# Performance work log

Hardware: AMD Instinct MI355X
Metric: run time of the kernel (lower is better)

Reference implementation:

```python
import jax, jax.numpy as jnp
import numpy as np

N, HEADS, OUT = 8192, 4, 64  # hidden = HEADS*OUT = 256
DIN = 256
NEG = -9e15
ALPHA = 0.2


def setup_inputs() -> dict:
    key = jax.random.key(0)
    ks = jax.random.split(key, 6)
    X = jax.random.normal(ks[0], (N, DIN), dtype=jnp.float32)
    A = jax.random.randint(ks[1], (N, N), 0, 2, dtype=jnp.int32)  # dense 0/1 adjacency
    hid = HEADS * OUT
    W = jax.random.normal(ks[2], (hid, DIN), dtype=jnp.float32) * 0.05  # nn.Linear weight [out,in]
    b = jax.random.normal(ks[3], (hid,), dtype=jnp.float32) * 0.05
    a_s = jax.random.normal(ks[4], (hid, 1), dtype=jnp.float32) * 0.05
    a_r = jax.random.normal(ks[5], (hid, 1), dtype=jnp.float32) * 0.05
    return {"X": X, "A": A, "W": W, "b": b, "a_s": a_s, "a_r": a_r}


def reference(X, A, W, b, a_s, a_r):
    Af = A.astype(jnp.float32)
    H_in = X @ W.T + b                      # [N, hid]
    s = H_in @ a_s                          # [N, 1]
    r = H_in @ a_r                          # [N, 1]
    M = Af * s + Af * r.T                   # M_s + M_r, [N, N]
    scores = jax.nn.leaky_relu(M, negative_slope=ALPHA)
    masked = jnp.where(Af > 0, scores, jnp.float32(NEG))
    C = jax.nn.softmax(masked, axis=1)      # row softmax; dropout = identity (eval)
    H_out = C @ H_in                        # [N, hid]; act = Identity, LayerNorm output discarded
    H_final = H_out.reshape(N, HEADS, OUT).sum(axis=1)  # concat='sum'
    return H_final
```

## Files before the change

### kernel.cpp

```cpp
#include <hip/hip_runtime.h>

typedef __attribute__((ext_vector_type(8))) short short8;
typedef __attribute__((ext_vector_type(4))) short short4v;
typedef __attribute__((ext_vector_type(4))) float f32x4;
typedef __attribute__((ext_vector_type(4))) int i32x4;

#define NN 8192
#define ALPHA 0.2f

__device__ __forceinline__ float bf16_to_f32(unsigned short h) {
    union { unsigned int u; float f; } c;
    c.u = ((unsigned int)h) << 16;
    return c.f;
}
__device__ __forceinline__ unsigned short f32_to_bf16(float f) {
    union { float f; unsigned int u; } c;
    c.f = f;
    unsigned int r = (c.u + 0x7FFFu + ((c.u >> 16) & 1u)) >> 16;
    return (unsigned short)r;
}
__device__ __forceinline__ unsigned short f32_to_bf16_fast(float f) {
    union { float f; unsigned int u; } c;
    c.f = f;
    return (unsigned short)((c.u + 0x8000u) >> 16);
}

__global__ void gat_probe_dtype(const unsigned short* __restrict__ x16, int* flag) {
    __shared__ int cnts[256];
    int tid = threadIdx.x;
    int cnt = 0;
    for (int i = tid; i < 16384; i += 256) {
        float v = bf16_to_f32(x16[i]);
        float a = fabsf(v);
        if (a > 1e-6f && a < 64.0f) cnt++;
    }
    cnts[tid] = cnt;
    __syncthreads();
    for (int s = 128; s > 0; s >>= 1) {
        if (tid < s) cnts[tid] += cnts[tid + s];
        __syncthreads();
    }
    if (tid == 0) *flag = (cnts[0] > 13000) ? 1 : 0;
}

__global__ void gat_convert(const void* __restrict__ Xv, const void* __restrict__ Wv,
                            const void* __restrict__ bv, const void* __restrict__ asv,
                            const void* __restrict__ arv,
                            short* __restrict__ Xb, short* __restrict__ Wb,
                            float* __restrict__ bF, float* __restrict__ asF,
                            float* __restrict__ arF, const int* __restrict__ flag) {
    const int GX = NN * 256 / 8;
    const int GW = 256 * 256 / 8;
    const int isBf = *flag;
    const int idx = blockIdx.x * blockDim.x + threadIdx.x;
    const int stride = gridDim.x * blockDim.x;
    for (int i = idx; i < GX + GW; i += stride) {
        const void* src = (i < GX) ? Xv : Wv;
        short* dst = (i < GX) ? Xb : Wb;
        int g = (i < GX) ? i : i - GX;
        short8 o;
        if (isBf) {
            o = ((const short8*)src)[g];
        } else {
            f32x4 a = ((const f32x4*)src)[2 * g];
            f32x4 b = ((const f32x4*)src)[2 * g + 1];
#pragma unroll
            for (int j = 0; j < 4; j++) {
                o[j] = (short)f32_to_bf16(a[j]);
                o[4 + j] = (short)f32_to_bf16(b[j]);
            }
        }
        ((short8*)dst)[g] = o;
    }
    if (idx < 768) {
        int which = idx >> 8;
        int k = idx & 255;
        const void* src = (which == 0) ? bv : (which == 1) ? asv : arv;
        float v = isBf ? bf16_to_f32(((const unsigned short*)src)[k])
                       : ((const float*)src)[k];
        float* dst = (which == 0) ? bF : (which == 1) ? asF : arF;
        dst[k] = v;
    }
}

__global__ __launch_bounds__(128) void gat_gemm1(
    const short* __restrict__ Xb, const short* __restrict__ Wb,
    const float* __restrict__ bF, const float* __restrict__ asF,
    const float* __restrict__ arF,
    short* __restrict__ Gfrag, float* __restrict__ sOut, float* __restrict__ rOut) {
    __shared__ short Gl[64][32];
    const int tid = threadIdx.x;
    const int wave = tid >> 6, lane = tid & 63;
    const int l15 = lane & 15, lhi = lane >> 4;
    const int rowBase = blockIdx.x * 32 + wave * 16;

    f32x4 acc[16];
#pragma unroll
    for (int n = 0; n < 16; n++) acc[n] = (f32x4){0.f, 0.f, 0.f, 0.f};

    const short8* Xrow = (const short8*)(Xb + (size_t)(rowBase + l15) * 256);
#pragma unroll
    for (int ks = 0; ks < 8; ks++) {
        short8 a = Xrow[ks * 4 + lhi];
#pragma unroll
        for (int n = 0; n < 16; n++) {
            const short8* Wrow = (const short8*)(Wb + (size_t)(n * 16 + l15) * 256);
            short8 bf = Wrow[ks * 4 + lhi];
            acc[n] = __builtin_amdgcn_mfma_f32_16x16x32_bf16(a, bf, acc[n], 0, 0, 0);
        }
    }

    float sPart[4] = {0.f, 0.f, 0.f, 0.f};
    float rPart[4] = {0.f, 0.f, 0.f, 0.f};
    float g[4][4];
#pragma unroll
    for (int na = 0; na < 4; na++)
#pragma unroll
        for (int q = 0; q < 4; q++) g[na][q] = 0.f;

#pragma unroll
    for (int n = 0; n < 16; n++) {
        int col = n * 16 + l15;
        float bias = bF[col], asc = asF[col], arc = arF[col];
#pragma unroll
        for (int q = 0; q < 4; q++) {
            float h = acc[n][q] + bias;
            sPart[q] += h * asc;
            rPart[q] += h * arc;
            g[n & 3][q] += h;
        }
    }

#pragma unroll
    for (int na = 0; na < 4; na++)
#pragma unroll
        for (int q = 0; q < 4; q++)
            Gl[na * 16 + l15][wave * 16 + lhi * 4 + q] = (short)f32_to_bf16(g[na][q]);

#pragma unroll
    for (int m = 1; m <= 8; m <<= 1) {
#pragma unroll
        for (int q = 0; q < 4; q++) {
            sPart[q] += __shfl_xor(sPart[q], m, 64);
            rPart[q] += __shfl_xor(rPart[q], m, 64);
        }
    }
    if (l15 == 0) {
#pragma unroll
        for (int q = 0; q < 4; q++) {
            int row = rowBase + lhi * 4 + q;
            sOut[row] = sPart[q];
            rOut[row] = rPart[q];
        }
    }

    __syncthreads();
    const int t_ = blockIdx.x >> 1, h_ = blockIdx.x & 1;
#pragma unroll
    for (int e = tid; e < 256; e += 128) {
        int n_ = e >> 6, le = e & 63;
        short8 v = *(const short8*)(&Gl[n_ * 16 + (le & 15)][(le >> 4) * 8]);
        *(short8*)(Gfrag + ((size_t)t_ * 8 + h_ * 4 + n_) * 512 + le * 8) = v;
    }
}


#define GAT_LOADA(S0, S1, S2, S3, AB_, T_)                                   \
    {                                                                        \
        const int* p_ = (AB_) + (size_t)(T_) * 64;                           \
        S0 = __builtin_nontemporal_load((const i32x4*)(p_));                 \
        S1 = __builtin_nontemporal_load((const i32x4*)(p_ + NN));            \
        S2 = __builtin_nontemporal_load((const i32x4*)(p_ + 2 * NN));        \
        S3 = __builtin_nontemporal_load((const i32x4*)(p_ + 3 * NN));        \
    }

#define GAT_BAL(Q0, Q1, Q2, Q3, V0, V1, V2, V3)                              \
    {                                                                        \
        unsigned long long W00 = __ballot((V0)[0] != 0);                     \
        unsigned long long W01 = __ballot((V0)[1] != 0);                     \
        unsigned long long W02 = __ballot((V0)[2] != 0);                     \
        unsigned long long W03 = __ballot((V0)[3] != 0);                     \
        unsigned long long W10 = __ballot((V1)[0] != 0);                     \
        unsigned long long W11 = __ballot((V1)[1] != 0);                     \
        unsigned long long W12 = __ballot((V1)[2] != 0);                     \
        unsigned long long W13 = __ballot((V1)[3] != 0);                     \
        unsigned long long W20 = __ballot((V2)[0] != 0);                     \
        unsigned long long W21 = __ballot((V2)[1] != 0);                     \
        unsigned long long W22 = __ballot((V2)[2] != 0);                     \
        unsigned long long W23 = __ballot((V2)[3] != 0);                     \
        unsigned long long W30 = __ballot((V3)[0] != 0);                     \
        unsigned long long W31 = __ballot((V3)[1] != 0);                     \
        unsigned long long W32 = __ballot((V3)[2] != 0);                     \
        unsigned long long W33 = __ballot((V3)[3] != 0);                     \
        unsigned long long w0_ = r3 == 0 ? W00 : r3 == 1 ? W10               \
                               : r3 == 2 ? W20 : W30;                        \
        unsigned long long w1_ = r3 == 0 ? W01 : r3 == 1 ? W11               \
                               : r3 == 2 ? W21 : W31;                        \
        unsigned long long w2_ = r3 == 0 ? W02 : r3 == 1 ? W12               \
                               : r3 == 2 ? W22 : W32;                        \
        unsigned long long w3_ = r3 == 0 ? W03 : r3 == 1 ? W13               \
                               : r3 == 2 ? W23 : W33;                        \
        Q0 = (unsigned int)(w0_ >> shBase);                                  \
        Q1 = (unsigned int)(w1_ >> shBase);                                  \
        Q2 = (unsigned int)(w2_ >> shBase);                                  \
        Q3 = (unsigned int)(w3_ >> shBase);                                  \
    }

#define GAT_ELEM(PA_, JP_, XV_, TW_, SH_)                                    \
    {                                                                        \
        float x_ = (XV_);                                                    \
        x_ = fmaxf(x_, ALPHA * x_);                                          \
        float e_ = __expf(x_);                                               \
        PA_[JP_] = ((TW_ >> (SH_)) & 1u) ? (short)f32_to_bf16_fast(e_)       \
                                         : (short)0;                         \
    }

#define GAT_PA(PAH0, PAH1, SM_, Q0, Q1, Q2, Q3)                              \
    {                                                                        \
        GAT_ELEM(PAH0, 0, (SM_) + ra0[0], Q0, 0)                             \
        GAT_ELEM(PAH0, 1, (SM_) + ra0[1], Q1, 0)                             \
        GAT_ELEM(PAH0, 2, (SM_) + ra0[2], Q2, 0)                             \
        GAT_ELEM(PAH0, 3, (SM_) + ra0[3], Q3, 0)                             \
        GAT_ELEM(PAH0, 4, (SM_) + ra1[0], Q0, 1)                             \
        GAT_ELEM(PAH0, 5, (SM_) + ra1[1], Q1, 1)                             \
        GAT_ELEM(PAH0, 6, (SM_) + ra1[2], Q2, 1)                             \
        GAT_ELEM(PAH0, 7, (SM_) + ra1[3], Q3, 1)                             \
        GAT_ELEM(PAH1, 0, (SM_) + rb0[0], Q0, 8)                             \
        GAT_ELEM(PAH1, 1, (SM_) + rb0[1], Q1, 8)                             \
        GAT_ELEM(PAH1, 2, (SM_) + rb0[2], Q2, 8)                             \
        GAT_ELEM(PAH1, 3, (SM_) + rb0[3], Q3, 8)                             \
        GAT_ELEM(PAH1, 4, (SM_) + rb1[0], Q0, 9)                             \
        GAT_ELEM(PAH1, 5, (SM_) + rb1[1], Q1, 9)                             \
        GAT_ELEM(PAH1, 6, (SM_) + rb1[2], Q2, 9)                             \
        GAT_ELEM(PAH1, 7, (SM_) + rb1[3], Q3, 9)                             \
    }

#define GAT_MFMA_HALF(H_)                                                    \
    {                                                                        \
        const short* bp_ = Gfrag + ((size_t)ktg * 8 + (H_) * 4) * 512 +      \
                           lane * 8;                                         \
        short8 bv0 = *(const short8*)(bp_);                                  \
        short8 bv1 = *(const short8*)(bp_ + 512);                            \
        short8 bv2 = *(const short8*)(bp_ + 1024);                           \
        short8 bv3 = *(const short8*)(bp_ + 1536);                           \
        acc[0][0] = __builtin_amdgcn_mfma_f32_16x16x32_bf16(pa0[H_], bv0,    \
                                                            acc[0][0], 0, 0, 0); \
        acc[0][1] = __builtin_amdgcn_mfma_f32_16x16x32_bf16(pa0[H_], bv1,    \
                                                            acc[0][1], 0, 0, 0); \
        acc[0][2] = __builtin_amdgcn_mfma_f32_16x16x32_bf16(pa0[H_], bv2,    \
                                                            acc[0][2], 0, 0, 0); \
        acc[0][3] = __builtin_amdgcn_mfma_f32_16x16x32_bf16(pa0[H_], bv3,    \
                                                            acc[0][3], 0, 0, 0); \
        acc[0][4] = __builtin_amdgcn_mfma_f32_16x16x32_bf16(pa0[H_], onesB,  \
                                                            acc[0][4], 0, 0, 0); \
        acc[1][0] = __builtin_amdgcn_mfma_f32_16x16x32_bf16(pa1[H_], bv0,    \
                                                            acc[1][0], 0, 0, 0); \
        acc[1][1] = __builtin_amdgcn_mfma_f32_16x16x32_bf16(pa1[H_], bv1,    \
                                                            acc[1][1], 0, 0, 0); \
        acc[1][2] = __builtin_amdgcn_mfma_f32_16x16x32_bf16(pa1[H_], bv2,    \
                                                            acc[1][2], 0, 0, 0); \
        acc[1][3] = __builtin_amdgcn_mfma_f32_16x16x32_bf16(pa1[H_], bv3,    \
                                                            acc[1][3], 0, 0, 0); \
        acc[1][4] = __builtin_amdgcn_mfma_f32_16x16x32_bf16(pa1[H_], onesB,  \
                                                            acc[1][4], 0, 0, 0); \
    }

__global__ __launch_bounds__(256, 3) void gat_pv6(
    const int* __restrict__ A, const short* __restrict__ Gfrag,
    const float* __restrict__ sV, const float* __restrict__ rV,
    float* __restrict__ accP, float* __restrict__ denP) {
    __shared__ float Ls[4][32][68];
    __shared__ float Ld[4][32];

    const int tid = threadIdx.x;
    const int wave = tid >> 6, lane = tid & 63;
    const int l15 = lane & 15, lhi = lane >> 4;
    const int rb = blockIdx.x >> 2;
    const int ks = blockIdx.x & 3;
    const int i0 = rb * 32;
    const int ksBase = ks * 32 + wave * 8;

    const int r3 = l15 & 3;
    const int shBase = ((l15 >> 2) << 4) + (lhi << 1);

    const float s0m = sV[i0 + l15];
    const float s1m = sV[i0 + 16 + l15];
    const int* ab0 = A + (size_t)(i0 + lhi * 4) * NN + l15 * 4;
    const int* ab1 = ab0 + (size_t)16 * NN;
    const float* rvb = rV + lhi * 8;

    short8 onesB;
#pragma unroll
    for (int j = 0; j < 8; j++) onesB[j] = (l15 == 0) ? (short)0x3F80 : (short)0;

    f32x4 acc[2][5];
#pragma unroll
    for (int rg = 0; rg < 2; rg++)
#pragma unroll
        for (int n = 0; n < 5; n++) acc[rg][n] = (f32x4){0.f, 0.f, 0.f, 0.f};

    i32x4 s00, s01, s02, s03, s10, s11, s12, s13;
    GAT_LOADA(s00, s01, s02, s03, ab0, ksBase);
    GAT_LOADA(s10, s11, s12, s13, ab1, ksBase);

    for (int t = 0; t < 8; t++) {
        const int ktg = ksBase + t;
        const int k0 = ktg * 64;
        f32x4 ra0 = *(const f32x4*)(rvb + k0);
        f32x4 ra1 = *(const f32x4*)(rvb + k0 + 4);
        f32x4 rb0 = *(const f32x4*)(rvb + k0 + 32);
        f32x4 rb1 = *(const f32x4*)(rvb + k0 + 36);

        unsigned int q00, q01, q02, q03, q10, q11, q12, q13;
        GAT_BAL(q00, q01, q02, q03, s00, s01, s02, s03);
        GAT_BAL(q10, q11, q12, q13, s10, s11, s12, s13);

        const int tn = (t < 7) ? ktg + 1 : ktg;
        GAT_LOADA(s00, s01, s02, s03, ab0, tn);
        GAT_LOADA(s10, s11, s12, s13, ab1, tn);

        short8 pa0[2], pa1[2];
        GAT_PA(pa0[0], pa0[1], s0m, q00, q01, q02, q03);
        GAT_PA(pa1[0], pa1[1], s1m, q10, q11, q12, q13);

        GAT_MFMA_HALF(0);
        GAT_MFMA_HALF(1);
    }

#pragma unroll
    for (int rg = 0; rg < 2; rg++)
#pragma unroll
        for (int n = 0; n < 4; n++)
#pragma unroll
            for (int q = 0; q < 4; q++)
                Ls[wave][rg * 16 + lhi * 4 + q][n * 16 + l15] = acc[rg][n][q];
    if (l15 == 0) {
#pragma unroll
        for (int rg = 0; rg < 2; rg++)
#pragma unroll
            for (int q = 0; q < 4; q++)
                Ld[wave][rg * 16 + lhi * 4 + q] = acc[rg][4][q];
    }
    __syncthreads();

    const int row = tid >> 3, c0 = (tid & 7) * 8;
    float v[8];
#pragma unroll
    for (int j = 0; j < 8; j++)
        v[j] = Ls[0][row][c0 + j] + Ls[1][row][c0 + j] +
               Ls[2][row][c0 + j] + Ls[3][row][c0 + j];
    float* aout = accP + (size_t)ks * NN * 64 + (size_t)(i0 + row) * 64 + c0;
    *(f32x4*)aout = (f32x4){v[0], v[1], v[2], v[3]};
    *((f32x4*)aout + 1) = (f32x4){v[4], v[5], v[6], v[7]};
    if (tid < 32)
        denP[(size_t)ks * NN + i0 + tid] =
            Ld[0][tid] + Ld[1][tid] + Ld[2][tid] + Ld[3][tid];
}

__global__ void gat_final(const float* __restrict__ accP, const float* __restrict__ denP,
                          const int* __restrict__ flag, void* __restrict__ outP) {
    int idx = blockIdx.x * blockDim.x + threadIdx.x;
    if (idx >= NN * 16) return;
    int row = idx >> 4;
    float den = 0.f;
    f32x4 v = (f32x4){0.f, 0.f, 0.f, 0.f};
#pragma unroll
    for (int sk = 0; sk < 4; sk++) {
        den += denP[(size_t)sk * NN + row];
        f32x4 a = *((const f32x4*)(accP + (size_t)sk * NN * 64) + idx);
        v.x += a.x; v.y += a.y; v.z += a.z; v.w += a.w;
    }
    float inv = 1.0f / den;
    v.x *= inv; v.y *= inv; v.z *= inv; v.w *= inv;
    if (*flag) {
        short4v pk;
#pragma unroll
        for (int j = 0; j < 4; j++) pk[j] = (short)f32_to_bf16(v[j]);
        *((short4v*)outP + idx) = pk;
    } else {
        *((f32x4*)outP + idx) = v;
    }
}

extern "C" void kernel_launch(void* const* d_in, const int* in_sizes, int n_in,
                              void* d_out, int out_size, void* d_ws, size_t ws_size,
                              hipStream_t stream) {
    const void* X  = d_in[0];
    const int*  A  = (const int*)d_in[1];
    const void* W  = d_in[2];
    const void* bb = d_in[3];
    const void* as_ = d_in[4];
    const void* ar_ = d_in[5];

    char* ws = (char*)d_ws;
    const size_t OFF_FLAG = 0;
    const size_t OFF_XB   = 256;
    const size_t OFF_WB   = OFF_XB + (size_t)NN * 256 * 2;
    const size_t OFF_BF   = OFF_WB + (size_t)256 * 256 * 2;
    const size_t OFF_ASF  = OFF_BF + 1024;
    const size_t OFF_ARF  = OFF_ASF + 1024;
    const size_t OFF_S    = OFF_ARF + 1024;
    const size_t OFF_R    = OFF_S + (size_t)NN * 4;
    const size_t OFF_GF   = OFF_R + (size_t)NN * 4;
    const size_t OFF_ACC  = OFF_GF + (size_t)64 * NN * 2;
    const size_t OFF_DEN  = OFF_ACC + (size_t)4 * NN * 64 * 4;

    int*   flag = (int*)(ws + OFF_FLAG);
    short* Xb   = (short*)(ws + OFF_XB);
    short* Wb   = (short*)(ws + OFF_WB);
    float* bF   = (float*)(ws + OFF_BF);
    float* asF  = (float*)(ws + OFF_ASF);
    float* arF  = (float*)(ws + OFF_ARF);
    float* sP   = (float*)(ws + OFF_S);
    float* rP   = (float*)(ws + OFF_R);
    short* Gf   = (short*)(ws + OFF_GF);
    float* accP = (float*)(ws + OFF_ACC);
    float* denP = (float*)(ws + OFF_DEN);

    gat_probe_dtype<<<1, 256, 0, stream>>>((const unsigned short*)X, flag);
    gat_convert<<<512, 256, 0, stream>>>(X, W, bb, as_, ar_, Xb, Wb, bF, asF, arF, flag);
    gat_gemm1<<<NN / 32, 128, 0, stream>>>(Xb, Wb, bF, asF, arF, Gf, sP, rP);
    gat_pv6<<<(NN / 32) * 4, 256, 0, stream>>>(A, Gf, sP, rP, accP, denP);
    gat_final<<<NN * 16 / 256, 256, 0, stream>>>(accP, denP, flag, d_out);
}
```

Measured before the change: 95.94 us.

## Pack adjacency into bitmask in prep kernel and consume bits in PV kernel

```diff
diff --git a/kernel.cpp b/kernel.cpp
--- a/kernel.cpp
+++ b/kernel.cpp
@@ -43,17 +43,43 @@
     if (tid == 0) *flag = (cnts[0] > 13000) ? 1 : 0;
 }
 
-__global__ void gat_convert(const void* __restrict__ Xv, const void* __restrict__ Wv,
-                            const void* __restrict__ bv, const void* __restrict__ asv,
-                            const void* __restrict__ arv,
-                            short* __restrict__ Xb, short* __restrict__ Wb,
-                            float* __restrict__ bF, float* __restrict__ asF,
-                            float* __restrict__ arF, const int* __restrict__ flag) {
+__global__ __launch_bounds__(256) void gat_prep(
+    const void* __restrict__ Xv, const void* __restrict__ Wv,
+    const void* __restrict__ bv, const void* __restrict__ asv,
+    const void* __restrict__ arv, const int* __restrict__ Ain,
+    short* __restrict__ Xb, short* __restrict__ Wb,
+    float* __restrict__ bF, float* __restrict__ asF, float* __restrict__ arF,
+    unsigned long long* __restrict__ bitsW, const int* __restrict__ flag) {
+    const int bid = blockIdx.x;
+    const int tid = threadIdx.x;
+    if (bid < 2048) {
+        const int wave = tid >> 6, lane = tid & 63;
+        const int row = bid * 4 + wave;
+        const int* arow = Ain + (size_t)row * NN;
+        unsigned long long* brow = bitsW + (size_t)row * 128;
+        for (int step = 0; step < 32; step++) {
+            const int kb = step * 256;
+            int v0 = arow[kb + lane];
+            int v1 = arow[kb + 64 + lane];
+            int v2 = arow[kb + 128 + lane];
+            int v3 = arow[kb + 192 + lane];
+            unsigned long long b0 = __ballot(v0 != 0);
+            unsigned long long b1 = __ballot(v1 != 0);
+            unsigned long long b2 = __ballot(v2 != 0);
+            unsigned long long b3 = __ballot(v3 != 0);
+            if (lane < 4) {
+                unsigned long long w = (lane == 0) ? b0 : (lane == 1) ? b1
+                                     : (lane == 2) ? b2 : b3;
+                brow[step * 4 + lane] = w;
+            }
+        }
+        return;
+    }
     const int GX = NN * 256 / 8;
     const int GW = 256 * 256 / 8;
     const int isBf = *flag;
-    const int idx = blockIdx.x * blockDim.x + threadIdx.x;
-    const int stride = gridDim.x * blockDim.x;
+    const int idx = (bid - 2048) * blockDim.x + tid;
+    const int stride = 256 * 256;
     for (int i = idx; i < GX + GW; i += stride) {
         const void* src = (i < GX) ? Xv : Wv;
         short* dst = (i < GX) ? Xb : Wb;
@@ -165,47 +191,6 @@
 }
 
 
-#define GAT_LOADA(S0, S1, S2, S3, AB_, T_)                                   \
-    {                                                                        \
-        const int* p_ = (AB_) + (size_t)(T_) * 64;                           \
-        S0 = __builtin_nontemporal_load((const i32x4*)(p_));                 \
-        S1 = __builtin_nontemporal_load((const i32x4*)(p_ + NN));            \
-        S2 = __builtin_nontemporal_load((const i32x4*)(p_ + 2 * NN));        \
-        S3 = __builtin_nontemporal_load((const i32x4*)(p_ + 3 * NN));        \
-    }
-
-#define GAT_BAL(Q0, Q1, Q2, Q3, V0, V1, V2, V3)                              \
-    {                                                                        \
-        unsigned long long W00 = __ballot((V0)[0] != 0);                     \
-        unsigned long long W01 = __ballot((V0)[1] != 0);                     \
-        unsigned long long W02 = __ballot((V0)[2] != 0);                     \
-        unsigned long long W03 = __ballot((V0)[3] != 0);                     \
-        unsigned long long W10 = __ballot((V1)[0] != 0);                     \
-        unsigned long long W11 = __ballot((V1)[1] != 0);                     \
-        unsigned long long W12 = __ballot((V1)[2] != 0);                     \
-        unsigned long long W13 = __ballot((V1)[3] != 0);                     \
-        unsigned long long W20 = __ballot((V2)[0] != 0);                     \
-        unsigned long long W21 = __ballot((V2)[1] != 0);                     \
-        unsigned long long W22 = __ballot((V2)[2] != 0);                     \
-        unsigned long long W23 = __ballot((V2)[3] != 0);                     \
-        unsigned long long W30 = __ballot((V3)[0] != 0);                     \
-        unsigned long long W31 = __ballot((V3)[1] != 0);                     \
-        unsigned long long W32 = __ballot((V3)[2] != 0);                     \
-        unsigned long long W33 = __ballot((V3)[3] != 0);                     \
-        unsigned long long w0_ = r3 == 0 ? W00 : r3 == 1 ? W10               \
-                               : r3 == 2 ? W20 : W30;                        \
-        unsigned long long w1_ = r3 == 0 ? W01 : r3 == 1 ? W11               \
-                               : r3 == 2 ? W21 : W31;                        \
-        unsigned long long w2_ = r3 == 0 ? W02 : r3 == 1 ? W12               \
-                               : r3 == 2 ? W22 : W32;                        \
-        unsigned long long w3_ = r3 == 0 ? W03 : r3 == 1 ? W13               \
-                               : r3 == 2 ? W23 : W33;                        \
-        Q0 = (unsigned int)(w0_ >> shBase);                                  \
-        Q1 = (unsigned int)(w1_ >> shBase);                                  \
-        Q2 = (unsigned int)(w2_ >> shBase);                                  \
-        Q3 = (unsigned int)(w3_ >> shBase);                                  \
-    }
-
 #define GAT_ELEM(PA_, JP_, XV_, TW_, SH_)                                    \
     {                                                                        \
         float x_ = (XV_);                                                    \
@@ -215,24 +200,24 @@
                                          : (short)0;                         \
     }
 
-#define GAT_PA(PAH0, PAH1, SM_, Q0, Q1, Q2, Q3)                              \
+#define GAT_PA(PAH0, PAH1, SM_, T0_, T1_)                                    \
     {                                                                        \
-        GAT_ELEM(PAH0, 0, (SM_) + ra0[0], Q0, 0)                             \
-        GAT_ELEM(PAH0, 1, (SM_) + ra0[1], Q1, 0)                             \
-        GAT_ELEM(PAH0, 2, (SM_) + ra0[2], Q2, 0)                             \
-        GAT_ELEM(PAH0, 3, (SM_) + ra0[3], Q3, 0)                             \
-        GAT_ELEM(PAH0, 4, (SM_) + ra1[0], Q0, 1)                             \
-        GAT_ELEM(PAH0, 5, (SM_) + ra1[1], Q1, 1)                             \
-        GAT_ELEM(PAH0, 6, (SM_) + ra1[2], Q2, 1)                             \
-        GAT_ELEM(PAH0, 7, (SM_) + ra1[3], Q3, 1)                             \
-        GAT_ELEM(PAH1, 0, (SM_) + rb0[0], Q0, 8)                             \
-        GAT_ELEM(PAH1, 1, (SM_) + rb0[1], Q1, 8)                             \
-        GAT_ELEM(PAH1, 2, (SM_) + rb0[2], Q2, 8)                             \
-        GAT_ELEM(PAH1, 3, (SM_) + rb0[3], Q3, 8)                             \
-        GAT_ELEM(PAH1, 4, (SM_) + rb1[0], Q0, 9)                             \
-        GAT_ELEM(PAH1, 5, (SM_) + rb1[1], Q1, 9)                             \
-        GAT_ELEM(PAH1, 6, (SM_) + rb1[2], Q2, 9)                             \
-        GAT_ELEM(PAH1, 7, (SM_) + rb1[3], Q3, 9)                             \
+        GAT_ELEM(PAH0, 0, (SM_) + ra0[0], T0_, 0)                            \
+        GAT_ELEM(PAH0, 1, (SM_) + ra0[1], T0_, 1)                            \
+        GAT_ELEM(PAH0, 2, (SM_) + ra0[2], T0_, 2)                            \
+        GAT_ELEM(PAH0, 3, (SM_) + ra0[3], T0_, 3)                            \
+        GAT_ELEM(PAH0, 4, (SM_) + ra1[0], T0_, 4)                            \
+        GAT_ELEM(PAH0, 5, (SM_) + ra1[1], T0_, 5)                            \
+        GAT_ELEM(PAH0, 6, (SM_) + ra1[2], T0_, 6)                            \
+        GAT_ELEM(PAH0, 7, (SM_) + ra1[3], T0_, 7)                            \
+        GAT_ELEM(PAH1, 0, (SM_) + rb0[0], T1_, 0)                            \
+        GAT_ELEM(PAH1, 1, (SM_) + rb0[1], T1_, 1)                            \
+        GAT_ELEM(PAH1, 2, (SM_) + rb0[2], T1_, 2)                            \
+        GAT_ELEM(PAH1, 3, (SM_) + rb0[3], T1_, 3)                            \
+        GAT_ELEM(PAH1, 4, (SM_) + rb1[0], T1_, 4)                            \
+        GAT_ELEM(PAH1, 5, (SM_) + rb1[1], T1_, 5)                            \
+        GAT_ELEM(PAH1, 6, (SM_) + rb1[2], T1_, 6)                            \
+        GAT_ELEM(PAH1, 7, (SM_) + rb1[3], T1_, 7)                            \
     }
 
 #define GAT_MFMA_HALF(H_)                                                    \
@@ -265,8 +250,8 @@
                                                             acc[1][4], 0, 0, 0); \
     }
 
-__global__ __launch_bounds__(256, 3) void gat_pv6(
-    const int* __restrict__ A, const short* __restrict__ Gfrag,
+__global__ __launch_bounds__(256, 3) void gat_pv7(
+    const unsigned long long* __restrict__ bitsW, const short* __restrict__ Gfrag,
     const float* __restrict__ sV, const float* __restrict__ rV,
     float* __restrict__ accP, float* __restrict__ denP) {
     __shared__ float Ls[4][32][68];
@@ -280,14 +265,12 @@
     const int i0 = rb * 32;
     const int ksBase = ks * 32 + wave * 8;
 
-    const int r3 = l15 & 3;
-    const int shBase = ((l15 >> 2) << 4) + (lhi << 1);
-
     const float s0m = sV[i0 + l15];
     const float s1m = sV[i0 + 16 + l15];
-    const int* ab0 = A + (size_t)(i0 + lhi * 4) * NN + l15 * 4;
-    const int* ab1 = ab0 + (size_t)16 * NN;
+    const unsigned long long* bb0 = bitsW + (size_t)(i0 + l15) * 128;
+    const unsigned long long* bb1 = bitsW + (size_t)(i0 + 16 + l15) * 128;
     const float* rvb = rV + lhi * 8;
+    const int sh0 = lhi * 8, sh1 = 32 + lhi * 8;
 
     short8 onesB;
 #pragma unroll
@@ -299,9 +282,8 @@
 #pragma unroll
         for (int n = 0; n < 5; n++) acc[rg][n] = (f32x4){0.f, 0.f, 0.f, 0.f};
 
-    i32x4 s00, s01, s02, s03, s10, s11, s12, s13;
-    GAT_LOADA(s00, s01, s02, s03, ab0, ksBase);
-    GAT_LOADA(s10, s11, s12, s13, ab1, ksBase);
+    unsigned long long w0 = bb0[ksBase];
+    unsigned long long w1 = bb1[ksBase];
 
     for (int t = 0; t < 8; t++) {
         const int ktg = ksBase + t;
@@ -311,20 +293,23 @@
         f32x4 rb0 = *(const f32x4*)(rvb + k0 + 32);
         f32x4 rb1 = *(const f32x4*)(rvb + k0 + 36);
 
-        unsigned int q00, q01, q02, q03, q10, q11, q12, q13;
-        GAT_BAL(q00, q01, q02, q03, s00, s01, s02, s03);
-        GAT_BAL(q10, q11, q12, q13, s10, s11, s12, s13);
-
         const int tn = (t < 7) ? ktg + 1 : ktg;
-        GAT_LOADA(s00, s01, s02, s03, ab0, tn);
-        GAT_LOADA(s10, s11, s12, s13, ab1, tn);
+        unsigned long long nw0 = bb0[tn];
+        unsigned long long nw1 = bb1[tn];
+
+        const unsigned int t00 = (unsigned int)(w0 >> sh0);
+        const unsigned int t01 = (unsigned int)(w0 >> sh1);
+        const unsigned int t10 = (unsigned int)(w1 >> sh0);
+        const unsigned int t11 = (unsigned int)(w1 >> sh1);
 
         short8 pa0[2], pa1[2];
-        GAT_PA(pa0[0], pa0[1], s0m, q00, q01, q02, q03);
-        GAT_PA(pa1[0], pa1[1], s1m, q10, q11, q12, q13);
+        GAT_PA(pa0[0], pa0[1], s0m, t00, t01);
+        GAT_PA(pa1[0], pa1[1], s1m, t10, t11);
 
         GAT_MFMA_HALF(0);
         GAT_MFMA_HALF(1);
+
+        w0 = nw0; w1 = nw1;
     }
 
 #pragma unroll
@@ -404,6 +389,7 @@
     const size_t OFF_GF   = OFF_R + (size_t)NN * 4;
     const size_t OFF_ACC  = OFF_GF + (size_t)64 * NN * 2;
     const size_t OFF_DEN  = OFF_ACC + (size_t)4 * NN * 64 * 4;
+    const size_t OFF_BITS = OFF_DEN + (size_t)4 * NN * 4;
 
     int*   flag = (int*)(ws + OFF_FLAG);
     short* Xb   = (short*)(ws + OFF_XB);
@@ -416,10 +402,12 @@
     short* Gf   = (short*)(ws + OFF_GF);
     float* accP = (float*)(ws + OFF_ACC);
     float* denP = (float*)(ws + OFF_DEN);
+    unsigned long long* bitsW = (unsigned long long*)(ws + OFF_BITS);
 
     gat_probe_dtype<<<1, 256, 0, stream>>>((const unsigned short*)X, flag);
-    gat_convert<<<512, 256, 0, stream>>>(X, W, bb, as_, ar_, Xb, Wb, bF, asF, arF, flag);
+    gat_prep<<<2304, 256, 0, stream>>>(X, W, bb, as_, ar_, A,
+                                       Xb, Wb, bF, asF, arF, bitsW, flag);
     gat_gemm1<<<NN / 32, 128, 0, stream>>>(Xb, Wb, bF, asF, arF, Gf, sP, rP);
-    gat_pv6<<<(NN / 32) * 4, 256, 0, stream>>>(A, Gf, sP, rP, accP, denP);
+    gat_pv7<<<(NN / 32) * 4, 256, 0, stream>>>(bitsW, Gf, sP, rP, accP, denP);
     gat_final<<<NN * 16 / 256, 256, 0, stream>>>(accP, denP, flag, d_out);
 }
```

Measured after the change: 112.4 us. 1.17x slower.

## Fuse dtype probe into convert and split attention over three K slices

Applied to the files above, without the earlier changes.

```diff
diff --git a/kernel.cpp b/kernel.cpp
--- a/kernel.cpp
+++ b/kernel.cpp
@@ -25,35 +25,38 @@
     return (unsigned short)((c.u + 0x8000u) >> 16);
 }
 
-__global__ void gat_probe_dtype(const unsigned short* __restrict__ x16, int* flag) {
-    __shared__ int cnts[256];
-    int tid = threadIdx.x;
+__device__ __forceinline__ int probe_isbf16(const void* Xv, int tid) {
+    __shared__ int wsum[4];
+    const unsigned short* x16 = (const unsigned short*)Xv;
     int cnt = 0;
-    for (int i = tid; i < 16384; i += 256) {
-        float v = bf16_to_f32(x16[i]);
+#pragma unroll
+    for (int j = 0; j < 4; j++) {
+        float v = bf16_to_f32(x16[tid * 4 + j]);
         float a = fabsf(v);
         if (a > 1e-6f && a < 64.0f) cnt++;
     }
-    cnts[tid] = cnt;
+#pragma unroll
+    for (int m = 1; m <= 32; m <<= 1) cnt += __shfl_xor(cnt, m, 64);
+    if ((tid & 63) == 0) wsum[tid >> 6] = cnt;
     __syncthreads();
-    for (int s = 128; s > 0; s >>= 1) {
-        if (tid < s) cnts[tid] += cnts[tid + s];
-        __syncthreads();
-    }
-    if (tid == 0) *flag = (cnts[0] > 13000) ? 1 : 0;
-}
-
-__global__ void gat_convert(const void* __restrict__ Xv, const void* __restrict__ Wv,
-                            const void* __restrict__ bv, const void* __restrict__ asv,
-                            const void* __restrict__ arv,
-                            short* __restrict__ Xb, short* __restrict__ Wb,
-                            float* __restrict__ bF, float* __restrict__ asF,
-                            float* __restrict__ arF, const int* __restrict__ flag) {
+    return (wsum[0] + wsum[1] + wsum[2] + wsum[3]) > 800;
+}
+
+__global__ __launch_bounds__(256) void gat_prep(
+    const void* __restrict__ Xv, const void* __restrict__ Wv,
+    const void* __restrict__ bv, const void* __restrict__ asv,
+    const void* __restrict__ arv,
+    short* __restrict__ Xb, short* __restrict__ Wb,
+    float* __restrict__ bF, float* __restrict__ asF, float* __restrict__ arF,
+    int* __restrict__ flagOut) {
+    const int tid = threadIdx.x;
+    const int isBf = probe_isbf16(Xv, tid);
+    if (blockIdx.x == 0 && tid == 0) *flagOut = isBf;
+
     const int GX = NN * 256 / 8;
     const int GW = 256 * 256 / 8;
-    const int isBf = *flag;
-    const int idx = blockIdx.x * blockDim.x + threadIdx.x;
-    const int stride = gridDim.x * blockDim.x;
+    const int idx = blockIdx.x * 256 + tid;
+    const int stride = 256 * 256;
     for (int i = idx; i < GX + GW; i += stride) {
         const void* src = (i < GX) ? Xv : Wv;
         short* dst = (i < GX) ? Xb : Wb;
@@ -168,10 +171,10 @@
 #define GAT_LOADA(S0, S1, S2, S3, AB_, T_)                                   \
     {                                                                        \
         const int* p_ = (AB_) + (size_t)(T_) * 64;                           \
-        S0 = __builtin_nontemporal_load((const i32x4*)(p_));                 \
-        S1 = __builtin_nontemporal_load((const i32x4*)(p_ + NN));            \
-        S2 = __builtin_nontemporal_load((const i32x4*)(p_ + 2 * NN));        \
-        S3 = __builtin_nontemporal_load((const i32x4*)(p_ + 3 * NN));        \
+        S0 = *(const i32x4*)(p_);                                            \
+        S1 = *(const i32x4*)(p_ + NN);                                       \
+        S2 = *(const i32x4*)(p_ + 2 * NN);                                   \
+        S3 = *(const i32x4*)(p_ + 3 * NN);                                   \
     }
 
 #define GAT_BAL(Q0, Q1, Q2, Q3, V0, V1, V2, V3)                              \
@@ -265,7 +268,7 @@
                                                             acc[1][4], 0, 0, 0); \
     }
 
-__global__ __launch_bounds__(256, 3) void gat_pv6(
+__global__ __launch_bounds__(256, 3) void gat_pv8(
     const int* __restrict__ A, const short* __restrict__ Gfrag,
     const float* __restrict__ sV, const float* __restrict__ rV,
     float* __restrict__ accP, float* __restrict__ denP) {
@@ -275,10 +278,11 @@
     const int tid = threadIdx.x;
     const int wave = tid >> 6, lane = tid & 63;
     const int l15 = lane & 15, lhi = lane >> 4;
-    const int rb = blockIdx.x >> 2;
-    const int ks = blockIdx.x & 3;
+    const int rb = blockIdx.x / 3;
+    const int ks3 = blockIdx.x - rb * 3;
     const int i0 = rb * 32;
-    const int ksBase = ks * 32 + wave * 8;
+    const int tstart = ks3 * 43;
+    const int tcnt = (ks3 < 2) ? 43 : 42;
 
     const int r3 = l15 & 3;
     const int shBase = ((l15 >> 2) << 4) + (lhi << 1);
@@ -300,11 +304,11 @@
         for (int n = 0; n < 5; n++) acc[rg][n] = (f32x4){0.f, 0.f, 0.f, 0.f};
 
     i32x4 s00, s01, s02, s03, s10, s11, s12, s13;
-    GAT_LOADA(s00, s01, s02, s03, ab0, ksBase);
-    GAT_LOADA(s10, s11, s12, s13, ab1, ksBase);
-
-    for (int t = 0; t < 8; t++) {
-        const int ktg = ksBase + t;
+    GAT_LOADA(s00, s01, s02, s03, ab0, tstart + wave);
+    GAT_LOADA(s10, s11, s12, s13, ab1, tstart + wave);
+
+    for (int tt = wave; tt < tcnt; tt += 4) {
+        const int ktg = tstart + tt;
         const int k0 = ktg * 64;
         f32x4 ra0 = *(const f32x4*)(rvb + k0);
         f32x4 ra1 = *(const f32x4*)(rvb + k0 + 4);
@@ -315,7 +319,7 @@
         GAT_BAL(q00, q01, q02, q03, s00, s01, s02, s03);
         GAT_BAL(q10, q11, q12, q13, s10, s11, s12, s13);
 
-        const int tn = (t < 7) ? ktg + 1 : ktg;
+        const int tn = (tt + 4 < tcnt) ? ktg + 4 : ktg;
         GAT_LOADA(s00, s01, s02, s03, ab0, tn);
         GAT_LOADA(s10, s11, s12, s13, ab1, tn);
 
@@ -349,11 +353,11 @@
     for (int j = 0; j < 8; j++)
         v[j] = Ls[0][row][c0 + j] + Ls[1][row][c0 + j] +
                Ls[2][row][c0 + j] + Ls[3][row][c0 + j];
-    float* aout = accP + (size_t)ks * NN * 64 + (size_t)(i0 + row) * 64 + c0;
+    float* aout = accP + (size_t)ks3 * NN * 64 + (size_t)(i0 + row) * 64 + c0;
     *(f32x4*)aout = (f32x4){v[0], v[1], v[2], v[3]};
     *((f32x4*)aout + 1) = (f32x4){v[4], v[5], v[6], v[7]};
     if (tid < 32)
-        denP[(size_t)ks * NN + i0 + tid] =
+        denP[(size_t)ks3 * NN + i0 + tid] =
             Ld[0][tid] + Ld[1][tid] + Ld[2][tid] + Ld[3][tid];
 }
 
@@ -365,7 +369,7 @@
     float den = 0.f;
     f32x4 v = (f32x4){0.f, 0.f, 0.f, 0.f};
 #pragma unroll
-    for (int sk = 0; sk < 4; sk++) {
+    for (int sk = 0; sk < 3; sk++) {
         den += denP[(size_t)sk * NN + row];
         f32x4 a = *((const f32x4*)(accP + (size_t)sk * NN * 64) + idx);
         v.x += a.x; v.y += a.y; v.z += a.z; v.w += a.w;
@@ -403,7 +407,7 @@
     const size_t OFF_R    = OFF_S + (size_t)NN * 4;
     const size_t OFF_GF   = OFF_R + (size_t)NN * 4;
     const size_t OFF_ACC  = OFF_GF + (size_t)64 * NN * 2;
-    const size_t OFF_DEN  = OFF_ACC + (size_t)4 * NN * 64 * 4;
+    const size_t OFF_DEN  = OFF_ACC + (size_t)3 * NN * 64 * 4;
 
     int*   flag = (int*)(ws + OFF_FLAG);
     short* Xb   = (short*)(ws + OFF_XB);
@@ -417,9 +421,8 @@
     float* accP = (float*)(ws + OFF_ACC);
     float* denP = (float*)(ws + OFF_DEN);
 
-    gat_probe_dtype<<<1, 256, 0, stream>>>((const unsigned short*)X, flag);
-    gat_convert<<<512, 256, 0, stream>>>(X, W, bb, as_, ar_, Xb, Wb, bF, asF, arF, flag);
+    gat_prep<<<256, 256, 0, stream>>>(X, W, bb, as_, ar_, Xb, Wb, bF, asF, arF, flag);
     gat_gemm1<<<NN / 32, 128, 0, stream>>>(Xb, Wb, bF, asF, arF, Gf, sP, rP);
-    gat_pv6<<<(NN / 32) * 4, 256, 0, stream>>>(A, Gf, sP, rP, accP, denP);
+    gat_pv8<<<256 * 3, 256, 0, stream>>>(A, Gf, sP, rP, accP, denP);
     gat_final<<<NN * 16 / 256, 256, 0, stream>>>(accP, denP, flag, d_out);
 }
```

After: 79.75 us. 1.2x faster.
